# Optimization experiments

Measured on AMD Instinct MI355X. Metric: run time of the kernel, lower is better.

Reference implementation:

```python
import jax, jax.numpy as jnp
import numpy as np

NUM_HEADS = 16
NEG_INF = -1e30


def setup_inputs() -> dict:
    key = jax.random.key(0)
    ks = jax.random.split(key, 12)
    T, B, E = 1024, 8, 1024
    H = NUM_HEADS
    hd = E // H
    gain = 1.0 / np.sqrt(2.0)
    # xavier_uniform bound for [E, E] weight
    bound = np.sqrt(6.0 / (E + E))
    inp = {
        "query": jax.random.normal(ks[0], (T, B, E), jnp.float32),
        "key": jax.random.normal(ks[1], (T, B, E), jnp.float32),
        "value": jax.random.normal(ks[2], (T, B, E), jnp.float32),
        "key_padding_mask": jnp.zeros((B, T), dtype=bool),  # no padding
        "attn_mask": jnp.triu(jnp.ones((T, T), dtype=bool), k=1),  # causal
        "Wq": jax.random.uniform(ks[3], (E, E), jnp.float32, -bound * gain, bound * gain),
        "bq": jnp.zeros((E,), jnp.float32),
        "Wk": jax.random.uniform(ks[4], (E, E), jnp.float32, -bound * gain, bound * gain),
        "bk": jnp.zeros((E,), jnp.float32),
        "Wv": jax.random.uniform(ks[5], (E, E), jnp.float32, -bound * gain, bound * gain),
        "bv": jnp.zeros((E,), jnp.float32),
        "Wo": jax.random.uniform(ks[6], (E, E), jnp.float32, -bound, bound),
        "bo": jnp.zeros((E,), jnp.float32),
    }
    return inp


def reference(query, key, value, key_padding_mask, attn_mask,
              Wq, bq, Wk, bk, Wv, bv, Wo, bo):
    T, B, E = query.shape
    H = NUM_HEADS
    hd = E // H
    scaling = hd ** -0.5
    S = key.shape[0]

    # projections (nn.Linear: x @ W.T + b)
    q = (query @ Wq.T + bq) * scaling          # [T, B, E]
    k = key @ Wk.T + bk                         # [S, B, E]
    v = value @ Wv.T + bv                       # [S, B, E]

    # -> [B*H, len, hd] (fairseq layout)
    q = q.reshape(T, B * H, hd).transpose(1, 0, 2)
    k = k.reshape(S, B * H, hd).transpose(1, 0, 2)
    v = v.reshape(S, B * H, hd).transpose(1, 0, 2)

    scores = jnp.einsum('nth,nsh->nts', q, k)   # [B*H, T, S]
    scores = jnp.where(attn_mask[None, :, :], NEG_INF, scores)
    scores = scores.reshape(B, H, T, S)
    scores = jnp.where(key_padding_mask[:, None, None, :], NEG_INF, scores)

    # fp32 softmax (matches softmax(..., dtype=torch.float32))
    weights = jax.nn.softmax(scores.astype(jnp.float32), axis=-1)  # [B, H, T, S]

    # dropout p=0.0 in eval -> identity
    probs = weights.reshape(B * H, T, S)
    attn = jnp.einsum('nts,nsh->nth', probs, v)  # [B*H, T, hd]
    attn = attn.transpose(1, 0, 2).reshape(T, B, E)
    attn = attn @ Wo.T + bo                      # [T, B, E]

    avg_weights = jnp.sum(weights, axis=1) / H   # [B, T, S]
    return attn, avg_weights, weights
```

## Files before the change

kernel.cpp:

```cpp
#include <hip/hip_runtime.h>
#include <hip/hip_bf16.h>
#include <stdint.h>

typedef unsigned short u16;
typedef __attribute__((ext_vector_type(8))) short bf16x8;
typedef __attribute__((ext_vector_type(4))) float f32x4;

#define LDS_AS __attribute__((address_space(3)))
#define GLB_AS __attribute__((address_space(1)))


__device__ __forceinline__ u16 f2bf(float f) {
  union { float f; uint32_t u; } v; v.f = f;
  uint32_t u = v.u;
  u += 0x7FFFu + ((u >> 16) & 1u);
  return (u16)(u >> 16);
}

__device__ __forceinline__ f32x4 mfma16(bf16x8 a, bf16x8 b, f32x4 c) {
  return __builtin_amdgcn_mfma_f32_16x16x32_bf16(a, b, c, 0, 0, 0);
}

__device__ __forceinline__ void gll16(const void* g, void* l) {
  __builtin_amdgcn_global_load_lds((const GLB_AS void*)(uintptr_t)g,
                                   (LDS_AS void*)(uintptr_t)l, 16, 0, 0);
}

__global__ __launch_bounds__(256) void k_cvt_all(
    const float* __restrict__ a0, const float* __restrict__ a1, const float* __restrict__ a2,
    const float* __restrict__ w0, const float* __restrict__ w1,
    const float* __restrict__ w2, const float* __restrict__ w3,
    u16* __restrict__ da0, u16* __restrict__ da1, u16* __restrict__ da2,
    u16* __restrict__ dw0, u16* __restrict__ dw1, u16* __restrict__ dw2, u16* __restrict__ dw3)
{
  int gid = blockIdx.x;
  const float* s; u16* d; int idx;
  if (gid < 24576) {
    int seg = gid >> 13; idx = gid & 8191;
    s = seg == 0 ? a0 : (seg == 1 ? a1 : a2);
    d = seg == 0 ? da0 : (seg == 1 ? da1 : da2);
  } else {
    int g2 = gid - 24576;
    int seg = g2 >> 10; idx = g2 & 1023;
    s = seg == 0 ? w0 : (seg == 1 ? w1 : (seg == 2 ? w2 : w3));
    d = seg == 0 ? dw0 : (seg == 1 ? dw1 : (seg == 2 ? dw2 : dw3));
  }
  int i = (idx * 256 + threadIdx.x) * 4;
  float4 v = *reinterpret_cast<const float4*>(s + i);
  ushort4 o;
  o.x = f2bf(v.x); o.y = f2bf(v.y); o.z = f2bf(v.z); o.w = f2bf(v.w);
  *reinterpret_cast<ushort4*>(d + i) = o;
}

__device__ __forceinline__ void gemm_core(
    const u16* __restrict__ A, const u16* __restrict__ Bw,
    const float* __restrict__ bias, void* __restrict__ outp, int mode)
{
  __shared__ u16 smem[2 * 128 * 64];
  u16* aLds = smem;
  u16* bLds = smem + 128 * 64;
  const int tid = threadIdx.x;
  const int w = tid >> 6, lane = tid & 63;
  const int fr = lane & 15, fh = lane >> 4;
  const int m0 = blockIdx.x * 128, n0 = blockIdx.y * 128;
  const int wr = w >> 1, wc = w & 1;
  const int srow = tid >> 3, scol = (tid & 7) * 8;

  f32x4 zero4 = {0.f, 0.f, 0.f, 0.f};
  f32x4 acc[4][4];
#pragma unroll
  for (int i = 0; i < 4; i++)
#pragma unroll
    for (int j = 0; j < 4; j++) acc[i][j] = zero4;

  const u16* ag = A + (size_t)(m0 + srow) * 1024 + scol;
  const u16* bg = Bw + (size_t)(n0 + srow) * 1024 + scol;

  for (int k0 = 0; k0 < 1024; k0 += 64) {
#pragma unroll
    for (int it = 0; it < 4; ++it) {
      gll16(ag + (size_t)it * 32 * 1024 + k0, aLds + it * 2048 + w * 512);
      gll16(bg + (size_t)it * 32 * 1024 + k0, bLds + it * 2048 + w * 512);
    }
    __syncthreads();
#pragma unroll
    for (int ks = 0; ks < 2; ++ks) {
      bf16x8 af[4], bfr[4];
#pragma unroll
      for (int mi = 0; mi < 4; mi++)
        af[mi] = *reinterpret_cast<const bf16x8*>(&aLds[(wr * 64 + mi * 16 + fr) * 64 + ks * 32 + fh * 8]);
#pragma unroll
      for (int nj = 0; nj < 4; nj++)
        bfr[nj] = *reinterpret_cast<const bf16x8*>(&bLds[(wc * 64 + nj * 16 + fr) * 64 + ks * 32 + fh * 8]);
#pragma unroll
      for (int mi = 0; mi < 4; mi++)
#pragma unroll
        for (int nj = 0; nj < 4; nj++)
          acc[mi][nj] = mfma16(af[mi], bfr[nj], acc[mi][nj]);
    }
    __syncthreads();
  }

  if (mode == 3) {
#pragma unroll
    for (int nj = 0; nj < 4; nj++) {
      int j = n0 + wc * 64 + nj * 16 + fr;
      float bj = bias[j];
#pragma unroll
      for (int mi = 0; mi < 4; mi++) {
#pragma unroll
        for (int r = 0; r < 4; r++) {
          int i = m0 + wr * 64 + mi * 16 + fh * 4 + r;
          ((float*)outp)[(size_t)i * 1024 + j] = acc[mi][nj][r] + bj;
        }
      }
    }
    return;
  }

  float scale = (mode == 0) ? 0.125f : 1.0f;
#pragma unroll
  for (int nj = 0; nj < 4; nj++) {
    int j = wc * 64 + nj * 16 + fr;
    float bj = bias[n0 + j];
#pragma unroll
    for (int mi = 0; mi < 4; mi++) {
#pragma unroll
      for (int r = 0; r < 4; r++) {
        int i = wr * 64 + mi * 16 + fh * 4 + r;
        smem[i * 128 + (j ^ ((i & 7) << 3))] = f2bf((acc[mi][nj][r] + bj) * scale);
      }
    }
  }
  __syncthreads();

  if (mode == 2) {
    int t0 = m0 >> 3;
#pragma unroll
    for (int rr2 = 0; rr2 < 4; ++rr2) {
      int rid = rr2 * 256 + tid;
      int b = rid & 7, jh = (rid >> 3) & 1, d = rid >> 4;
      int j_loc = jh * 64 + d;
      u16 tmp[16];
#pragma unroll
      for (int tt = 0; tt < 16; ++tt) {
        int i_loc = tt * 8 + b;
        tmp[tt] = smem[i_loc * 128 + (j_loc ^ ((i_loc & 7) << 3))];
      }
      int n = b * 16 + ((n0 + j_loc) >> 6);
      int d_ = (n0 + j_loc) & 63;
      u16* dst = (u16*)outp + (size_t)n * 65536 + (size_t)d_ * 1024 + t0;
      *reinterpret_cast<uint4*>(dst)     = *reinterpret_cast<const uint4*>(&tmp[0]);
      *reinterpret_cast<uint4*>(dst + 8) = *reinterpret_cast<const uint4*>(&tmp[8]);
    }
  } else {
#pragma unroll
    for (int it = 0; it < 8; ++it) {
      int g = w * 512 + it * 64 + lane;
      int i = g >> 4;
      int cg = (g & 15) * 8;
      uint4 v = *reinterpret_cast<const uint4*>(&smem[i * 128 + (cg ^ ((i & 7) << 3))]);
      int t = (m0 + i) >> 3, b = i & 7;
      int jg = n0 + cg;
      int h = jg >> 6, d = jg & 63;
      *reinterpret_cast<uint4*>(&((u16*)outp)[((size_t)((b * 16 + h) * 1024 + t)) * 64 + d]) = v;
    }
  }
}

__global__ __launch_bounds__(256) void k_gemm_qkv(
    const u16* __restrict__ xq, const u16* __restrict__ xk, const u16* __restrict__ xv,
    const u16* __restrict__ wq, const u16* __restrict__ wk, const u16* __restrict__ wv,
    const float* __restrict__ bq, const float* __restrict__ bk, const float* __restrict__ bv,
    u16* __restrict__ qo, u16* __restrict__ ko, u16* __restrict__ vto)
{
  int z = blockIdx.z;
  const u16* A = z == 0 ? xq : (z == 1 ? xk : xv);
  const u16* Bw = z == 0 ? wq : (z == 1 ? wk : wv);
  const float* bias = z == 0 ? bq : (z == 1 ? bk : bv);
  u16* o = z == 0 ? qo : (z == 1 ? ko : vto);
  gemm_core(A, Bw, bias, o, z);
}

__global__ __launch_bounds__(256) void k_gemm_o(
    const u16* __restrict__ A, const u16* __restrict__ Bw,
    const float* __restrict__ bias, float* __restrict__ outp)
{
  gemm_core(A, Bw, bias, outp, 3);
}

__device__ __forceinline__ void attn_step(
    const u16* lds_k, u16* lds_p, const bf16x8 (&vf)[2][4],
    int sb, int tb_, int w, int fr, int fh,
    bf16x8 qf0, bf16x8 qf1,
    f32x4 (&oacc)[4], float (&m4)[4], float (&l4)[4])
{
  int t0 = tb_ * 64 + w * 16;
  f32x4 dd[4];
#pragma unroll
  for (int ss = 0; ss < 4; ++ss) {
    int row = ss * 16 + fr;
    const u16* kr = lds_k + row * 64;
    int c0 = (fh * 16) ^ ((row & 7) << 4);
    int c1 = (64 + fh * 16) ^ ((row & 7) << 4);
    bf16x8 kf0 = *reinterpret_cast<const bf16x8*>(kr + (c0 >> 1));
    bf16x8 kf1 = *reinterpret_cast<const bf16x8*>(kr + (c1 >> 1));
    f32x4 z = {0.f, 0.f, 0.f, 0.f};
    z = mfma16(qf0, kf0, z);
    dd[ss] = mfma16(qf1, kf1, z);
  }
  if (sb == tb_) {
#pragma unroll
    for (int ss = 0; ss < 4; ++ss) {
      int s_c = sb * 64 + ss * 16 + fr;
#pragma unroll
      for (int r = 0; r < 4; ++r)
        if (s_c > t0 + fh * 4 + r) dd[ss][r] = -3.0e38f;
    }
  }
  float mn[4], scale[4];
#pragma unroll
  for (int r = 0; r < 4; ++r) {
    float bm = fmaxf(fmaxf(dd[0][r], dd[1][r]), fmaxf(dd[2][r], dd[3][r]));
#pragma unroll
    for (int bmk = 1; bmk < 16; bmk <<= 1)
      bm = fmaxf(bm, __shfl_xor(bm, bmk, 64));
    mn[r] = fmaxf(m4[r], bm);
    scale[r] = __expf(m4[r] - mn[r]);
    m4[r] = mn[r];
  }
#pragma unroll
  for (int ss = 0; ss < 4; ++ss) {
#pragma unroll
    for (int r = 0; r < 4; ++r) {
      float p = __expf(dd[ss][r] - mn[r]);
      dd[ss][r] = p;
      int row = fh * 4 + r;
      int cb = ((ss * 16 + fr) * 2) ^ ((row & 7) << 4);
      lds_p[row * 64 + (cb >> 1)] = f2bf(p);
    }
  }
#pragma unroll
  for (int r = 0; r < 4; ++r) {
    float s = (dd[0][r] + dd[1][r]) + (dd[2][r] + dd[3][r]);
#pragma unroll
    for (int bmk = 1; bmk < 16; bmk <<= 1)
      s += __shfl_xor(s, bmk, 64);
    l4[r] = l4[r] * scale[r] + s;
#pragma unroll
    for (int db = 0; db < 4; ++db) oacc[db][r] *= scale[r];
  }
  asm volatile("s_waitcnt lgkmcnt(0)" ::: "memory");
  __builtin_amdgcn_sched_barrier(0);
#pragma unroll
  for (int ks = 0; ks < 2; ++ks) {
    int pc = (ks * 64 + fh * 16) ^ ((fr & 7) << 4);
    bf16x8 pa = *reinterpret_cast<const bf16x8*>(lds_p + fr * 64 + (pc >> 1));
#pragma unroll
    for (int db = 0; db < 4; ++db)
      oacc[db] = mfma16(pa, vf[ks][db], oacc[db]);
  }
}

__global__ __launch_bounds__(256) void k_attn(
    const u16* __restrict__ qb, const u16* __restrict__ kb, const u16* __restrict__ vt,
    float* __restrict__ m_ws, float* __restrict__ l_ws, u16* __restrict__ attn_pre)
{
  __shared__ u16 kT[2][64 * 64];
  __shared__ u16 pT[4][16 * 64];
  int tid = threadIdx.x, w = tid >> 6, lane = tid & 63;
  int fr = lane & 15, fh = lane >> 4;
  int n = blockIdx.x, j = blockIdx.y;
  int tbH = 15 - j, tbL = j;
  const u16* kb_n = kb + (size_t)n * 1024 * 64;
  const u16* vt_n = vt + (size_t)n * 64 * 1024;

  bf16x8 qfH0, qfH1, qfL0, qfL1;
  {
    const u16* q = qb + ((size_t)n * 1024 + tbH * 64 + w * 16 + fr) * 64;
    qfH0 = *reinterpret_cast<const bf16x8*>(q + fh * 8);
    qfH1 = *reinterpret_cast<const bf16x8*>(q + 32 + fh * 8);
    q = qb + ((size_t)n * 1024 + tbL * 64 + w * 16 + fr) * 64;
    qfL0 = *reinterpret_cast<const bf16x8*>(q + fh * 8);
    qfL1 = *reinterpret_cast<const bf16x8*>(q + 32 + fh * 8);
  }
  f32x4 oaccH[4], oaccL[4];
  float mH[4], lH[4], mL[4], lL[4];
#pragma unroll
  for (int i = 0; i < 4; ++i) {
    oaccH[i] = (f32x4){0.f, 0.f, 0.f, 0.f};
    oaccL[i] = (f32x4){0.f, 0.f, 0.f, 0.f};
    mH[i] = -3.0e38f; lH[i] = 0.f; mL[i] = -3.0e38f; lL[i] = 0.f;
  }

  auto stage = [&](int buf, int sb) {
#pragma unroll
    for (int it = 0; it < 2; ++it) {
      int rbase = w * 16 + it * 8;
      int row = rbase + (lane >> 3);
      int colb = ((lane & 7) * 16) ^ ((lane >> 3) << 4);
      const u16* src = kb_n + ((size_t)(sb * 64 + row)) * 64 + (colb >> 1);
      gll16(src, &kT[buf][rbase * 64]);
    }
  };

  stage(0, 0);
  asm volatile("s_waitcnt vmcnt(0)" ::: "memory");
  __syncthreads();
  int cur = 0;
  for (int sb = 0; sb <= tbH; ++sb) {
    if (sb < tbH) stage(cur ^ 1, sb + 1);
    bf16x8 vf[2][4];
#pragma unroll
    for (int ks = 0; ks < 2; ++ks)
#pragma unroll
      for (int db = 0; db < 4; ++db)
        vf[ks][db] = *reinterpret_cast<const bf16x8*>(
            vt_n + ((size_t)(db * 16 + fr)) * 1024 + sb * 64 + ks * 32 + fh * 8);
    attn_step(kT[cur], pT[w], vf, sb, tbH, w, fr, fh, qfH0, qfH1, oaccH, mH, lH);
    if (sb <= tbL)
      attn_step(kT[cur], pT[w], vf, sb, tbL, w, fr, fh, qfL0, qfL1, oaccL, mL, lL);
    asm volatile("s_waitcnt vmcnt(0)" ::: "memory");
    __syncthreads();
    cur ^= 1;
  }

  int b_ = n >> 4, h_ = n & 15;
  {
    int t0 = tbH * 64 + w * 16;
    if (fr == 0) {
#pragma unroll
      for (int r = 0; r < 4; ++r) {
        m_ws[n * 1024 + t0 + fh * 4 + r] = mH[r];
        l_ws[n * 1024 + t0 + fh * 4 + r] = lH[r];
      }
    }
#pragma unroll
    for (int db = 0; db < 4; ++db)
#pragma unroll
      for (int r = 0; r < 4; ++r)
        attn_pre[((size_t)((t0 + fh * 4 + r) * 8 + b_)) * 1024 + h_ * 64 + db * 16 + fr] =
            f2bf(oaccH[db][r] / lH[r]);
  }
  {
    int t0 = tbL * 64 + w * 16;
    if (fr == 0) {
#pragma unroll
      for (int r = 0; r < 4; ++r) {
        m_ws[n * 1024 + t0 + fh * 4 + r] = mL[r];
        l_ws[n * 1024 + t0 + fh * 4 + r] = lL[r];
      }
    }
#pragma unroll
    for (int db = 0; db < 4; ++db)
#pragma unroll
      for (int r = 0; r < 4; ++r)
        attn_pre[((size_t)((t0 + fh * 4 + r) * 8 + b_)) * 1024 + h_ * 64 + db * 16 + fr] =
            f2bf(oaccL[db][r] / lL[r]);
  }
}

__global__ __launch_bounds__(512) void k_weights(
    const u16* __restrict__ qb, const u16* __restrict__ kb,
    const float* __restrict__ m_ws, const float* __restrict__ l_ws,
    float* __restrict__ wout, float* __restrict__ avg)
{
  __shared__ u16 kT[2][512 * 64];
  const float L2E = 1.4426950408889634f;
  int pid = blockIdx.x;
  int b = pid & 7, pr = pid >> 3;
  int tid = threadIdx.x;
  int w = tid >> 6, lane = tid & 63, fr = lane & 15, fh = lane >> 4;
  f32x4 zero4 = {0.f, 0.f, 0.f, 0.f};

  int pA = pr, pB = 63 - pr;
  int t0A = pA * 16, t0B = pB * 16;

  f32x4 avgA[8], avgB[8];
#pragma unroll
  for (int i = 0; i < 8; ++i) { avgA[i] = zero4; avgB[i] = zero4; }

  const int srow8 = lane >> 3;
  const int scolb = ((lane & 7) * 16) ^ (srow8 << 4);

  auto stage = [&](int buf, int cc) {
    const u16* kb_n = kb + (size_t)(b * 16 + (cc >> 1)) * 65536;
    int base = (cc & 1) * 512;
#pragma unroll
    for (int j = 0; j < 8; ++j) {
      int rbase = j * 64 + w * 8;
      const u16* src = kb_n + ((size_t)(base + rbase + srow8)) * 64 + (scolb >> 1);
      gll16(src, &kT[buf][rbase * 64]);
    }
  };

  stage(0, 0);
  int cur = 0;

  bf16x8 qA0, qA1, qB0, qB1;
  float cA = 0.f, cB = 0.f;
  float* wrowA = nullptr;
  float* wrowB = nullptr;

  for (int h = 0; h < 16; ++h) {
    int n = b * 16 + h;
#pragma unroll
    for (int kh = 0; kh < 2; ++kh) {
      int cc = h * 2 + kh;
      __builtin_amdgcn_s_barrier();
      __builtin_amdgcn_sched_barrier(0);
      if (cc < 31) stage(cur ^ 1, cc + 1);
      __builtin_amdgcn_sched_barrier(0);
      if (kh == 0) {
        if (h == 0) { asm volatile("s_waitcnt vmcnt(8)" ::: "memory"); }
        else        { asm volatile("s_waitcnt vmcnt(16)" ::: "memory"); }
      } else {
        if (h == 15) { asm volatile("s_waitcnt vmcnt(16)" ::: "memory"); }
        else         { asm volatile("s_waitcnt vmcnt(24)" ::: "memory"); }
      }
      __builtin_amdgcn_s_barrier();
      __builtin_amdgcn_sched_barrier(0);

      if (kh == 0) {
        const u16* qrA = qb + ((size_t)n * 1024 + t0A + fr) * 64;
        const u16* qrB = qb + ((size_t)n * 1024 + t0B + fr) * 64;
        qA0 = *reinterpret_cast<const bf16x8*>(qrA + fh * 8);
        qA1 = *reinterpret_cast<const bf16x8*>(qrA + 32 + fh * 8);
        qB0 = *reinterpret_cast<const bf16x8*>(qrB + fh * 8);
        qB1 = *reinterpret_cast<const bf16x8*>(qrB + 32 + fh * 8);
        cA = -m_ws[n * 1024 + t0A + fr] * L2E - __log2f(l_ws[n * 1024 + t0A + fr]);
        cB = -m_ws[n * 1024 + t0B + fr] * L2E - __log2f(l_ws[n * 1024 + t0B + fr]);
        wrowA = wout + ((size_t)n << 20) + ((size_t)t0A << 10);
        wrowB = wout + ((size_t)n << 20) + ((size_t)t0B << 10);
      }

      const u16* kbuf_l = kT[cur];
#pragma unroll
      for (int i = 0; i < 4; ++i) {
        int sl = w + 8 * i;
        int sg = kh * 32 + sl;
        f32x4 wvA = zero4, wvB = zero4;
        if (sg <= pB) {
          int rowl = sl * 16 + fr;
          const u16* kr = &kbuf_l[rowl * 64];
          int c0 = (fh * 16) ^ ((rowl & 7) << 4);
          int c1 = (64 + fh * 16) ^ ((rowl & 7) << 4);
          bf16x8 kf0 = *reinterpret_cast<const bf16x8*>(kr + (c0 >> 1));
          bf16x8 kf1 = *reinterpret_cast<const bf16x8*>(kr + (c1 >> 1));
          if (sg <= pA) {
            f32x4 dd = zero4;
            dd = mfma16(kf0, qA0, dd);
            dd = mfma16(kf1, qA1, dd);
#pragma unroll
            for (int rr = 0; rr < 4; ++rr) {
              bool valid = (sg < pA) | (fh * 4 + rr <= fr);
              wvA[rr] = valid ? __builtin_amdgcn_exp2f(dd[rr] * L2E + cA) : 0.f;
            }
          }
          {
            f32x4 dd = zero4;
            dd = mfma16(kf0, qB0, dd);
            dd = mfma16(kf1, qB1, dd);
#pragma unroll
            for (int rr = 0; rr < 4; ++rr) {
              bool valid = (sg < pB) | (fh * 4 + rr <= fr);
              wvB[rr] = valid ? __builtin_amdgcn_exp2f(dd[rr] * L2E + cB) : 0.f;
            }
          }
        }
        avgA[kh * 4 + i] += wvA;
        avgB[kh * 4 + i] += wvB;
        __builtin_nontemporal_store(wvA,
            reinterpret_cast<f32x4*>(wrowA + (size_t)fr * 1024 + sg * 16 + fh * 4));
        __builtin_nontemporal_store(wvB,
            reinterpret_cast<f32x4*>(wrowB + (size_t)fr * 1024 + sg * 16 + fh * 4));
      }
      cur ^= 1;
    }
  }

  float* arowA = avg + (((size_t)b << 10) + t0A) * 1024;
  float* arowB = avg + (((size_t)b << 10) + t0B) * 1024;
#pragma unroll
  for (int i = 0; i < 8; ++i) {
    int sg = (i >> 2) * 32 + (w + 8 * (i & 3));
    f32x4 vA = avgA[i], vB = avgB[i];
#pragma unroll
    for (int rr = 0; rr < 4; ++rr) { vA[rr] *= 0.0625f; vB[rr] *= 0.0625f; }
    __builtin_nontemporal_store(vA,
        reinterpret_cast<f32x4*>(arowA + (size_t)fr * 1024 + sg * 16 + fh * 4));
    __builtin_nontemporal_store(vB,
        reinterpret_cast<f32x4*>(arowB + (size_t)fr * 1024 + sg * 16 + fh * 4));
  }
}

extern "C" void kernel_launch(void* const* d_in, const int* in_sizes, int n_in,
                              void* d_out, int out_size, void* d_ws, size_t ws_size,
                              hipStream_t stream)
{
  const float* query = (const float*)d_in[0];
  const float* key_  = (const float*)d_in[1];
  const float* value = (const float*)d_in[2];
  const float* Wq = (const float*)d_in[5];
  const float* bq = (const float*)d_in[6];
  const float* Wk = (const float*)d_in[7];
  const float* bk = (const float*)d_in[8];
  const float* Wv = (const float*)d_in[9];
  const float* bv = (const float*)d_in[10];
  const float* Wo = (const float*)d_in[11];
  const float* bo = (const float*)d_in[12];

  char* ws = (char*)d_ws;
  size_t off = 0;
  auto alloc = [&](size_t bytes) { char* p = ws + off; off += (bytes + 255) & ~255ull; return p; };

  u16* xq   = (u16*)alloc(8192ull * 1024 * 2);
  u16* xk   = (u16*)alloc(8192ull * 1024 * 2);
  u16* xv   = (u16*)alloc(8192ull * 1024 * 2);
  u16* wqb  = (u16*)alloc(1024ull * 1024 * 2);
  u16* wkb  = (u16*)alloc(1024ull * 1024 * 2);
  u16* wvb  = (u16*)alloc(1024ull * 1024 * 2);
  u16* wob  = (u16*)alloc(1024ull * 1024 * 2);
  u16* qbuf = (u16*)alloc(128ull * 1024 * 64 * 2);
  u16* kbuf = (u16*)alloc(128ull * 1024 * 64 * 2);
  u16* vtb  = (u16*)alloc(128ull * 64 * 1024 * 2);
  u16* apre = (u16*)alloc(8192ull * 1024 * 2);
  float* mws = (float*)alloc(128ull * 1024 * 4);
  float* lws = (float*)alloc(128ull * 1024 * 4);

  float* out_attn = (float*)d_out;
  float* out_avg  = out_attn + 8388608;
  float* out_w    = out_avg + 8388608;

  k_cvt_all<<<28672, 256, 0, stream>>>(query, key_, value, Wq, Wk, Wv, Wo,
                                       xq, xk, xv, wqb, wkb, wvb, wob);

  k_gemm_qkv<<<dim3(64, 8, 3), 256, 0, stream>>>(xq, xk, xv, wqb, wkb, wvb,
                                                 bq, bk, bv, qbuf, kbuf, vtb);

  k_attn<<<dim3(128, 8), 256, 0, stream>>>(qbuf, kbuf, vtb, mws, lws, apre);
  k_weights<<<256, 512, 0, stream>>>(qbuf, kbuf, mws, lws, out_w, out_avg);
  k_gemm_o<<<dim3(64, 8), 256, 0, stream>>>(apre, wob, bo, out_attn);
}
```

Before: 364.5 us.

## Load K fragments directly from global memory in weights kernel, drop LDS staging

Removes the double-buffered LDS staging of K tiles (global_load_lds plus barriers and waitcnt) in the attention-weights kernel. Each wave now reads its K fragments straight from global memory and loops over all 8 key slabs per head in one pass. This eliminates the 128 KB of shared memory and the block-wide barriers, which may raise occupancy and reduce sync stalls. In exchange, K reads are no longer prefetched ahead and rely on cache hits, and the 16-byte loads are not swizzled.

```diff
diff --git a/kernel.cpp b/kernel.cpp
--- a/kernel.cpp
+++ b/kernel.cpp
@@ -365,7 +365,6 @@
     const float* __restrict__ m_ws, const float* __restrict__ l_ws,
     float* __restrict__ wout, float* __restrict__ avg)
 {
-  __shared__ u16 kT[2][512 * 64];
   const float L2E = 1.4426950408889634f;
   int pid = blockIdx.x;
   int b = pid & 7, pr = pid >> 3;
@@ -380,102 +379,55 @@
 #pragma unroll
   for (int i = 0; i < 8; ++i) { avgA[i] = zero4; avgB[i] = zero4; }
 
-  const int srow8 = lane >> 3;
-  const int scolb = ((lane & 7) * 16) ^ (srow8 << 4);
-
-  auto stage = [&](int buf, int cc) {
-    const u16* kb_n = kb + (size_t)(b * 16 + (cc >> 1)) * 65536;
-    int base = (cc & 1) * 512;
-#pragma unroll
-    for (int j = 0; j < 8; ++j) {
-      int rbase = j * 64 + w * 8;
-      const u16* src = kb_n + ((size_t)(base + rbase + srow8)) * 64 + (scolb >> 1);
-      gll16(src, &kT[buf][rbase * 64]);
-    }
-  };
-
-  stage(0, 0);
-  int cur = 0;
-
-  bf16x8 qA0, qA1, qB0, qB1;
-  float cA = 0.f, cB = 0.f;
-  float* wrowA = nullptr;
-  float* wrowB = nullptr;
-
   for (int h = 0; h < 16; ++h) {
     int n = b * 16 + h;
-#pragma unroll
-    for (int kh = 0; kh < 2; ++kh) {
-      int cc = h * 2 + kh;
-      __builtin_amdgcn_s_barrier();
-      __builtin_amdgcn_sched_barrier(0);
-      if (cc < 31) stage(cur ^ 1, cc + 1);
-      __builtin_amdgcn_sched_barrier(0);
-      if (kh == 0) {
-        if (h == 0) { asm volatile("s_waitcnt vmcnt(8)" ::: "memory"); }
-        else        { asm volatile("s_waitcnt vmcnt(16)" ::: "memory"); }
-      } else {
-        if (h == 15) { asm volatile("s_waitcnt vmcnt(16)" ::: "memory"); }
-        else         { asm volatile("s_waitcnt vmcnt(24)" ::: "memory"); }
-      }
-      __builtin_amdgcn_s_barrier();
-      __builtin_amdgcn_sched_barrier(0);
-
-      if (kh == 0) {
-        const u16* qrA = qb + ((size_t)n * 1024 + t0A + fr) * 64;
-        const u16* qrB = qb + ((size_t)n * 1024 + t0B + fr) * 64;
-        qA0 = *reinterpret_cast<const bf16x8*>(qrA + fh * 8);
-        qA1 = *reinterpret_cast<const bf16x8*>(qrA + 32 + fh * 8);
-        qB0 = *reinterpret_cast<const bf16x8*>(qrB + fh * 8);
-        qB1 = *reinterpret_cast<const bf16x8*>(qrB + 32 + fh * 8);
-        cA = -m_ws[n * 1024 + t0A + fr] * L2E - __log2f(l_ws[n * 1024 + t0A + fr]);
-        cB = -m_ws[n * 1024 + t0B + fr] * L2E - __log2f(l_ws[n * 1024 + t0B + fr]);
-        wrowA = wout + ((size_t)n << 20) + ((size_t)t0A << 10);
-        wrowB = wout + ((size_t)n << 20) + ((size_t)t0B << 10);
-      }
-
-      const u16* kbuf_l = kT[cur];
-#pragma unroll
-      for (int i = 0; i < 4; ++i) {
-        int sl = w + 8 * i;
-        int sg = kh * 32 + sl;
-        f32x4 wvA = zero4, wvB = zero4;
-        if (sg <= pB) {
-          int rowl = sl * 16 + fr;
-          const u16* kr = &kbuf_l[rowl * 64];
-          int c0 = (fh * 16) ^ ((rowl & 7) << 4);
-          int c1 = (64 + fh * 16) ^ ((rowl & 7) << 4);
-          bf16x8 kf0 = *reinterpret_cast<const bf16x8*>(kr + (c0 >> 1));
-          bf16x8 kf1 = *reinterpret_cast<const bf16x8*>(kr + (c1 >> 1));
-          if (sg <= pA) {
-            f32x4 dd = zero4;
-            dd = mfma16(kf0, qA0, dd);
-            dd = mfma16(kf1, qA1, dd);
-#pragma unroll
-            for (int rr = 0; rr < 4; ++rr) {
-              bool valid = (sg < pA) | (fh * 4 + rr <= fr);
-              wvA[rr] = valid ? __builtin_amdgcn_exp2f(dd[rr] * L2E + cA) : 0.f;
-            }
-          }
-          {
-            f32x4 dd = zero4;
-            dd = mfma16(kf0, qB0, dd);
-            dd = mfma16(kf1, qB1, dd);
-#pragma unroll
-            for (int rr = 0; rr < 4; ++rr) {
-              bool valid = (sg < pB) | (fh * 4 + rr <= fr);
-              wvB[rr] = valid ? __builtin_amdgcn_exp2f(dd[rr] * L2E + cB) : 0.f;
-            }
+    const u16* kb_n = kb + (size_t)n * 65536;
+    const u16* qrA = qb + ((size_t)n * 1024 + t0A + fr) * 64;
+    const u16* qrB = qb + ((size_t)n * 1024 + t0B + fr) * 64;
+    bf16x8 qA0 = *reinterpret_cast<const bf16x8*>(qrA + fh * 8);
+    bf16x8 qA1 = *reinterpret_cast<const bf16x8*>(qrA + 32 + fh * 8);
+    bf16x8 qB0 = *reinterpret_cast<const bf16x8*>(qrB + fh * 8);
+    bf16x8 qB1 = *reinterpret_cast<const bf16x8*>(qrB + 32 + fh * 8);
+    float cA = -m_ws[n * 1024 + t0A + fr] * L2E - __log2f(l_ws[n * 1024 + t0A + fr]);
+    float cB = -m_ws[n * 1024 + t0B + fr] * L2E - __log2f(l_ws[n * 1024 + t0B + fr]);
+    float* wrowA = wout + ((size_t)n << 20) + ((size_t)t0A << 10);
+    float* wrowB = wout + ((size_t)n << 20) + ((size_t)t0B << 10);
+
+#pragma unroll
+    for (int i = 0; i < 8; ++i) {
+      int sg = w + 8 * i;
+      f32x4 wvA = zero4, wvB = zero4;
+      if (sg <= pB) {
+        const u16* krow = kb_n + ((size_t)(sg * 16 + fr)) * 64;
+        bf16x8 kf0 = *reinterpret_cast<const bf16x8*>(krow + fh * 8);
+        bf16x8 kf1 = *reinterpret_cast<const bf16x8*>(krow + 32 + fh * 8);
+        if (sg <= pA) {
+          f32x4 dd = zero4;
+          dd = mfma16(kf0, qA0, dd);
+          dd = mfma16(kf1, qA1, dd);
+#pragma unroll
+          for (int rr = 0; rr < 4; ++rr) {
+            bool valid = (sg < pA) | (fh * 4 + rr <= fr);
+            wvA[rr] = valid ? __builtin_amdgcn_exp2f(dd[rr] * L2E + cA) : 0.f;
           }
         }
-        avgA[kh * 4 + i] += wvA;
-        avgB[kh * 4 + i] += wvB;
-        __builtin_nontemporal_store(wvA,
-            reinterpret_cast<f32x4*>(wrowA + (size_t)fr * 1024 + sg * 16 + fh * 4));
-        __builtin_nontemporal_store(wvB,
-            reinterpret_cast<f32x4*>(wrowB + (size_t)fr * 1024 + sg * 16 + fh * 4));
-      }
-      cur ^= 1;
+        {
+          f32x4 dd = zero4;
+          dd = mfma16(kf0, qB0, dd);
+          dd = mfma16(kf1, qB1, dd);
+#pragma unroll
+          for (int rr = 0; rr < 4; ++rr) {
+            bool valid = (sg < pB) | (fh * 4 + rr <= fr);
+            wvB[rr] = valid ? __builtin_amdgcn_exp2f(dd[rr] * L2E + cB) : 0.f;
+          }
+        }
+      }
+      avgA[i] += wvA;
+      avgB[i] += wvB;
+      __builtin_nontemporal_store(wvA,
+          reinterpret_cast<f32x4*>(wrowA + (size_t)fr * 1024 + sg * 16 + fh * 4));
+      __builtin_nontemporal_store(wvB,
+          reinterpret_cast<f32x4*>(wrowB + (size_t)fr * 1024 + sg * 16 + fh * 4));
     }
   }
 
@@ -483,7 +435,7 @@
   float* arowB = avg + (((size_t)b << 10) + t0B) * 1024;
 #pragma unroll
   for (int i = 0; i < 8; ++i) {
-    int sg = (i >> 2) * 32 + (w + 8 * (i & 3));
+    int sg = w + 8 * i;
     f32x4 vA = avgA[i], vB = avgB[i];
 #pragma unroll
     for (int rr = 0; rr < 4; ++rr) { vA[rr] *= 0.0625f; vB[rr] *= 0.0625f; }
```

After: 375.9 us. +3.1%, slower.
